# Optimization experiments

Measured on AMD Instinct MI355X. Metric: run time of the kernel, lower is better.

Reference implementation:

```python
import jax, jax.numpy as jnp
import numpy as np
import math

V, D, L, FF, H, DH, W, DM, T, B = 32000, 1024, 4, 4096, 16, 64, 256, 64, 1024, 1


def rms_norm(x, w):
    return x * jax.lax.rsqrt(jnp.mean(x * x, axis=-1, keepdims=True) + 1e-6) * w


def setup_inputs() -> dict:
    key = jax.random.key(0)
    ks = jax.random.split(key, 16)
    s = 0.02
    return {
        "x": jax.random.randint(ks[0], (B, T), 0, V),
        "embed": jax.random.normal(ks[1], (V, D), jnp.float32) * s,
        "ln_in_w": jnp.ones((D,), jnp.float32),
        "ln1_w": jnp.ones((L, D), jnp.float32),
        "lnd_w": jnp.ones((L, D), jnp.float32),
        "qkv_w": jax.random.normal(ks[2], (L, 3 * H * DH, D), jnp.float32) * s,
        "swa_out_w": jax.random.normal(ks[3], (L, D, H * DH), jnp.float32) * s,
        "k_w": jax.random.normal(ks[4], (L, H * DM, D), jnp.float32) * s,
        "v_w": jax.random.normal(ks[5], (L, H * DM, D), jnp.float32) * s,
        "q_w": jax.random.normal(ks[6], (L, H * DM, D), jnp.float32) * s,
        "beta_w": jax.random.normal(ks[7], (L, H, D), jnp.float32) * s,
        "mem_out_w": jax.random.normal(ks[8], (L, D, H * DM), jnp.float32) * s,
        "gate_w": jax.random.normal(ks[9], (L, D, D), jnp.float32) * s,
        "comb_w": jax.random.normal(ks[10], (L, D, D), jnp.float32) * s,
        "ln2_w": jnp.ones((L, D), jnp.float32),
        "wg": jax.random.normal(ks[11], (L, FF, D), jnp.float32) * s,
        "wu": jax.random.normal(ks[12], (L, FF, D), jnp.float32) * s,
        "wo": jax.random.normal(ks[13], (L, D, FF), jnp.float32) * s,
        "ln_out_w": jnp.ones((D,), jnp.float32),
    }


def _swa(h1, qkv_w, out_w):
    # h1: [B,T,D]
    qkv = jnp.einsum('btd,ed->bte', h1, qkv_w)  # [B,T,3*H*DH]
    q, k, v = jnp.split(qkv, 3, axis=-1)
    q = q.reshape(h1.shape[0], T, H, DH).transpose(0, 2, 1, 3)
    k = k.reshape(h1.shape[0], T, H, DH).transpose(0, 2, 1, 3)
    v = v.reshape(h1.shape[0], T, H, DH).transpose(0, 2, 1, 3)
    scores = jnp.einsum('bhqd,bhkd->bhqk', q, k) * (DH ** -0.5)
    pos = jnp.arange(T)
    dist = pos[:, None] - pos[None, :]
    allowed = (dist >= 0) & (dist < W)  # causal sliding window
    scores = jnp.where(allowed[None, None], scores, -jnp.inf)
    attn = jax.nn.softmax(scores, axis=-1)
    out = jnp.einsum('bhqk,bhkd->bhqd', attn, v)
    out = out.transpose(0, 2, 1, 3).reshape(h1.shape[0], T, H * DH)
    return jnp.einsum('bte,de->btd', out, out_w)


def _delta(h2, k_w, v_w, q_w, beta_w, mem_out_w):
    Bv = h2.shape[0]
    proj = lambda w: jnp.einsum('btd,ed->bte', h2, w).reshape(Bv, T, H, DM).transpose(0, 2, 1, 3)
    keys, values, queries = proj(k_w), proj(v_w), proj(q_w)
    beta = jax.nn.sigmoid(jnp.einsum('btd,hd->bht', h2, beta_w))  # [B,H,T]
    keys = keys / jnp.maximum(jnp.linalg.norm(keys, axis=-1, keepdims=True), 1e-12)
    queries = queries / jnp.maximum(jnp.linalg.norm(queries, axis=-1, keepdims=True), 1e-12)
    log_retain = jnp.log(1.0 - beta + 1e-8)
    cum_log = jnp.cumsum(log_retain, axis=-1)  # [B,H,T]
    log_decay = cum_log[..., :, None] - cum_log[..., None, :]  # [B,H,T,T]
    causal = jnp.triu(jnp.ones((T, T), dtype=bool))  # matches torch.triu mask in source
    decay = jnp.exp(jnp.minimum(log_decay, 0.0)) * causal
    kq = jnp.einsum('bhid,bhjd->bhij', queries, keys) / math.sqrt(DM)
    weights = kq * decay
    out = jnp.einsum('bhij,bhjd->bhid', weights, values)
    out = out + beta[..., None] * values
    out = out.transpose(0, 2, 1, 3).reshape(Bv, T, H * DM)
    return jnp.einsum('bte,de->btd', out, mem_out_w)


def reference(x, embed, ln_in_w, ln1_w, lnd_w, qkv_w, swa_out_w, k_w, v_w, q_w,
              beta_w, mem_out_w, gate_w, comb_w, ln2_w, wg, wu, wo, ln_out_w):
    h = rms_norm(embed[x], ln_in_w)  # [B,T,D]
    for l in range(L):
        h1 = rms_norm(h, ln1_w[l])
        h2 = rms_norm(h, lnd_w[l])
        local = _swa(h1, qkv_w[l], swa_out_w[l])
        global_ctx = _delta(h2, k_w[l], v_w[l], q_w[l], beta_w[l], mem_out_w[l])
        gate = jax.nn.sigmoid(jnp.einsum('btd,ed->bte', h1, gate_w[l]))
        mixed = jnp.einsum('btd,ed->bte', gate * local + (1.0 - gate) * global_ctx, comb_w[l])
        h = h + mixed
        hn = rms_norm(h, ln2_w[l])
        ffn = jnp.einsum('btf,df->btd', jax.nn.silu(jnp.einsum('btd,fd->btf', hn, wg[l])) * jnp.einsum('btd,fd->btf', hn, wu[l]), wo[l])
        h = h + ffn
    logits = jnp.einsum('btd,vd->btv', rms_norm(h, ln_out_w), embed)  # tied head
    return logits
```

## Files before the change

kernel.cpp:

```cpp
#include <hip/hip_runtime.h>

typedef unsigned short u16;
typedef unsigned int   u32;
typedef __attribute__((ext_vector_type(8))) __bf16 bfv8;
typedef __attribute__((ext_vector_type(4))) float  f32x4;
typedef __attribute__((ext_vector_type(4))) u32    u32x4;

__device__ __forceinline__ u16 f2bf(float f){
  u32 u = __builtin_bit_cast(u32, f);
  return (u16)((u + 0x7FFFu + ((u >> 16) & 1u)) >> 16);
}
__device__ __forceinline__ float bf2f(u16 b){
  return __builtin_bit_cast(float, ((u32)b) << 16);
}
__device__ __forceinline__ u32 pk2(float a, float b){
  return (u32)f2bf(a) | ((u32)f2bf(b) << 16);
}
__device__ __forceinline__ float wsum(float v){
  #pragma unroll
  for (int m = 32; m > 0; m >>= 1) v += __shfl_xor(v, m, 64);
  return v;
}
__device__ __forceinline__ void gload16(const void* g, void* l){
  __builtin_amdgcn_global_load_lds((const __attribute__((address_space(1))) void*)g,
                                   (__attribute__((address_space(3))) void*)l, 16, 0, 0);
}

struct CBatch { const float* s[12]; long long p4[13]; u16* dst; };
__global__ __launch_bounds__(256) void flm_conv(CBatch cb)
{
  const int seg = blockIdx.y;
  const long long base = cb.p4[seg];
  const long long n8 = (cb.p4[seg + 1] - base) >> 1;
  const f32x4* __restrict__ src = (const f32x4*)cb.s[seg];
  u32x4* __restrict__ dst = (u32x4*)cb.dst + (base >> 1);
  for (long long i = (long long)blockIdx.x * 256 + threadIdx.x; i < n8;
       i += (long long)gridDim.x * 256){
    f32x4 v0 = __builtin_nontemporal_load(src + 2*i);
    f32x4 v1 = __builtin_nontemporal_load(src + 2*i + 1);
    u32x4 p;
    p.x = pk2(v0.x, v0.y); p.y = pk2(v0.z, v0.w);
    p.z = pk2(v1.x, v1.y); p.w = pk2(v1.z, v1.w);
    __builtin_nontemporal_store(p, dst + i);
  }
}

struct GDesc {
  const u16* A; const float* Bw; float* Cf; u16* Cb;
  int lda, ldb, ldc, kbeg, kend, blk0, epi, pad;
};
struct GBatch { GDesc d[6]; int ng, total; };

template<bool BW>
__global__ __launch_bounds__(512) void flm_mgemm(GBatch gb)
{
  constexpr int LDK = BW ? 64 : 72;
  __shared__ u16 sA[128][LDK];
  __shared__ u16 sB[128][LDK];
  const int tid = threadIdx.x, lane = tid & 63, w = tid >> 6;

  const int T = gb.total, bid = blockIdx.x;
  const int q8 = T >> 3, r8 = T & 7, xc = bid & 7, of = bid >> 3;
  const int lin = (xc < r8 ? xc * (q8 + 1) : r8 * (q8 + 1) + (xc - r8) * q8) + of;
  int di = 0;
  #pragma unroll
  for (int i = 1; i < 6; i++) if (i < gb.ng && lin >= gb.d[i].blk0) di = i;
  const GDesc g = gb.d[di];
  const int local = lin - g.blk0;
  const int row0 = (local & 7) * 128;
  const int col0 = (local >> 3) * 128;
  const int wr = (w >> 2) * 64, wc = (w & 3) * 32;

  f32x4 acc[4][2];
  #pragma unroll
  for (int m = 0; m < 4; m++)
    #pragma unroll
    for (int n = 0; n < 2; n++)
      acc[m][n] = (f32x4){0.f, 0.f, 0.f, 0.f};

  const int csw = ((lane & 7) ^ (lane >> 3)) * 8;
  const u16* B16 = (const u16*)g.Bw;

  for (int k0 = g.kbeg; k0 < g.kend; k0 += 64){
    if constexpr (BW){
      const u16* a0 = g.A + (size_t)(row0 + w*16 + (lane>>3)) * g.lda + k0 + csw;
      const u16* b0 = B16 + (size_t)(col0 + w*16 + (lane>>3)) * g.ldb + k0 + csw;
      gload16(a0,                     &sA[w*16    ][0]);
      gload16(a0 + (size_t)8*g.lda,   &sA[w*16 + 8][0]);
      gload16(b0,                     &sB[w*16    ][0]);
      gload16(b0 + (size_t)8*g.ldb,   &sB[w*16 + 8][0]);
    } else {
      #pragma unroll
      for (int i = 0; i < 2; i++){
        int idx = tid + i * 512;
        int r = idx >> 3, c = (idx & 7) * 8;
        *(uint4*)&sA[r][c] = *(const uint4*)(g.A + (size_t)(row0 + r) * g.lda + k0 + c);
      }
      #pragma unroll
      for (int i = 0; i < 4; i++){
        int idx = tid + i * 512;
        int r = idx >> 4, c = (idx & 15) * 4;
        float4 v = *(const float4*)(g.Bw + (size_t)(col0 + r) * g.ldb + k0 + c);
        uint2 p; p.x = pk2(v.x, v.y); p.y = pk2(v.z, v.w);
        *(uint2*)&sB[r][c] = p;
      }
    }
    __syncthreads();
    #pragma unroll
    for (int kk = 0; kk < 2; kk++){
      bfv8 af[4], bfr[2];
      #pragma unroll
      for (int m = 0; m < 4; m++){
        int row = wr + m*16 + (lane & 15);
        if constexpr (BW){
          int slot = (kk*4 + (lane >> 4)) ^ (row & 7);
          af[m] = *(const bfv8*)((const char*)sA + row*128 + slot*16);
        } else {
          af[m] = *(const bfv8*)&sA[row][kk*32 + (lane >> 4) * 8];
        }
      }
      #pragma unroll
      for (int n = 0; n < 2; n++){
        int row = wc + n*16 + (lane & 15);
        if constexpr (BW){
          int slot = (kk*4 + (lane >> 4)) ^ (row & 7);
          bfr[n] = *(const bfv8*)((const char*)sB + row*128 + slot*16);
        } else {
          bfr[n] = *(const bfv8*)&sB[row][kk*32 + (lane >> 4) * 8];
        }
      }
      #pragma unroll
      for (int m = 0; m < 4; m++)
        #pragma unroll
        for (int n = 0; n < 2; n++)
          acc[m][n] = __builtin_amdgcn_mfma_f32_16x16x32_bf16(af[m], bfr[n], acc[m][n], 0, 0, 0);
    }
    __syncthreads();
  }

  #pragma unroll
  for (int m = 0; m < 4; m++){
    int rbase = row0 + wr + m*16 + (lane >> 4) * 4;
    #pragma unroll
    for (int n = 0; n < 2; n++){
      int col = col0 + wc + n*16 + (lane & 15);
      #pragma unroll
      for (int j = 0; j < 4; j++){
        float v = acc[m][n][j];
        size_t o = (size_t)(rbase + j) * g.ldc + col;
        switch (g.epi){
          case 0: g.Cf[o] = v; break;
          case 1: g.Cb[o] = f2bf(v); break;
          default: atomicAdd(&g.Cf[o], v); break;
        }
      }
    }
  }
}

__global__ __launch_bounds__(256) void flm_mix(
    const float* __restrict__ gr, const float* __restrict__ lo,
    const float* __restrict__ gl, u16* __restrict__ o)
{
  int i = blockIdx.x * 256 + threadIdx.x;
  float4 gv = ((const float4*)gr)[i];
  float4 lv = ((const float4*)lo)[i];
  float4 bv = ((const float4*)gl)[i];
  float sx = 1.f/(1.f+expf(-gv.x)), sy = 1.f/(1.f+expf(-gv.y));
  float sz = 1.f/(1.f+expf(-gv.z)), sw = 1.f/(1.f+expf(-gv.w));
  uint2 p;
  p.x = pk2(sx*lv.x + (1.f-sx)*bv.x, sy*lv.y + (1.f-sy)*bv.y);
  p.y = pk2(sz*lv.z + (1.f-sz)*bv.z, sw*lv.w + (1.f-sw)*bv.w);
  ((uint2*)o)[i] = p;
}

__global__ __launch_bounds__(256) void flm_silu(
    const u16* __restrict__ gg, const u16* __restrict__ uu, u16* __restrict__ o)
{
  int i = blockIdx.x * 256 + threadIdx.x;
  uint2 gv = ((const uint2*)gg)[i];
  uint2 uv = ((const uint2*)uu)[i];
  float g0 = bf2f((u16)gv.x), g1 = bf2f((u16)(gv.x >> 16));
  float g2 = bf2f((u16)gv.y), g3 = bf2f((u16)(gv.y >> 16));
  float u0 = bf2f((u16)uv.x), u1 = bf2f((u16)(uv.x >> 16));
  float u2 = bf2f((u16)uv.y), u3 = bf2f((u16)(uv.y >> 16));
  float a = g0 / (1.f + expf(-g0)) * u0;
  float b = g1 / (1.f + expf(-g1)) * u1;
  float c = g2 / (1.f + expf(-g2)) * u2;
  float d = g3 / (1.f + expf(-g3)) * u3;
  uint2 p; p.x = pk2(a, b); p.y = pk2(c, d);
  ((uint2*)o)[i] = p;
}

__global__ __launch_bounds__(256) void flm_embed(
    const int* __restrict__ x, const float* __restrict__ embed,
    const float* __restrict__ w, float* __restrict__ h)
{
  int t = blockIdx.x, tid = threadIdx.x;
  int tok = x[t];
  float4 v = ((const float4*)(embed + (size_t)tok * 1024))[tid];
  float ss = v.x*v.x + v.y*v.y + v.z*v.z + v.w*v.w;
  ss = wsum(ss);
  __shared__ float red[4];
  if ((tid & 63) == 0) red[tid >> 6] = ss;
  __syncthreads();
  float inv = rsqrtf((red[0]+red[1]+red[2]+red[3]) * (1.f/1024.f) + 1e-6f);
  float4 wv = ((const float4*)w)[tid];
  float4 o; o.x = v.x*inv*wv.x; o.y = v.y*inv*wv.y; o.z = v.z*inv*wv.z; o.w = v.w*inv*wv.w;
  ((float4*)(h + (size_t)t * 1024))[tid] = o;
}

__global__ __launch_bounds__(256) void flm_rms(
    const float* __restrict__ h, const float* __restrict__ w1, const float* __restrict__ w2,
    u16* __restrict__ o1, u16* __restrict__ o2)
{
  int t = blockIdx.x, tid = threadIdx.x;
  float4 v = ((const float4*)(h + (size_t)t * 1024))[tid];
  float ss = v.x*v.x + v.y*v.y + v.z*v.z + v.w*v.w;
  ss = wsum(ss);
  __shared__ float red[4];
  if ((tid & 63) == 0) red[tid >> 6] = ss;
  __syncthreads();
  float inv = rsqrtf((red[0]+red[1]+red[2]+red[3]) * (1.f/1024.f) + 1e-6f);
  {
    float4 wv = ((const float4*)w1)[tid];
    uint2 p; p.x = pk2(v.x*inv*wv.x, v.y*inv*wv.y); p.y = pk2(v.z*inv*wv.z, v.w*inv*wv.w);
    ((uint2*)(o1 + (size_t)t * 1024))[tid] = p;
  }
  if (o2 != nullptr){
    float4 wv = ((const float4*)w2)[tid];
    uint2 p; p.x = pk2(v.x*inv*wv.x, v.y*inv*wv.y); p.y = pk2(v.z*inv*wv.z, v.w*inv*wv.w);
    ((uint2*)(o2 + (size_t)t * 1024))[tid] = p;
  }
}

__global__ __launch_bounds__(64) void flm_betanorm(
    const u16* __restrict__ h2, const float* __restrict__ bw, float* __restrict__ beta,
    u16* __restrict__ keys, u16* __restrict__ queries)
{
  int t = blockIdx.x, lane = threadIdx.x;
  float hv[16];
  #pragma unroll
  for (int i = 0; i < 16; i++) hv[i] = bf2f(h2[(size_t)t*1024 + i*64 + lane]);
  for (int h = 0; h < 16; h++){
    float p = 0.f;
    #pragma unroll
    for (int i = 0; i < 16; i++) p += hv[i] * bw[h*1024 + i*64 + lane];
    p = wsum(p);
    if (lane == 0) beta[t*16 + h] = 1.f / (1.f + expf(-p));
  }
  #pragma unroll
  for (int h = 0; h < 16; h++){
    size_t idx = (size_t)t * 1024 + h * 64 + lane;
    float v = bf2f(keys[idx]);
    float nrm = fmaxf(sqrtf(wsum(v * v)), 1e-12f);
    keys[idx] = f2bf(v / nrm);
    float q = bf2f(queries[idx]);
    float qn = fmaxf(sqrtf(wsum(q * q)), 1e-12f);
    queries[idx] = f2bf(q / qn);
  }
}

__global__ __launch_bounds__(256) void flm_attn(
    const u16* __restrict__ qkv,
    const u16* __restrict__ keys, const u16* __restrict__ values, const u16* __restrict__ queries,
    const float* __restrict__ beta, u16* __restrict__ aout, u16* __restrict__ dout)
{
  __shared__ u16 sK[64][72];
  __shared__ u16 sVt[64][72];
  __shared__ u16 sP[4][16][72];
  const int tid = threadIdx.x, lane = tid & 63, w = tid >> 6;
  const int bx = blockIdx.x, h = blockIdx.y;
  const int base = h * 64;
  const int ri = w*16 + (lane>>4)*4;

  if (bx < 16){
    const int qt = bx;
    bfv8 aq[2];
    {
      int qrow = qt*64 + w*16 + (lane & 15);
      #pragma unroll
      for (int kk = 0; kk < 2; kk++)
        aq[kk] = *(const bfv8*)(qkv + (size_t)qrow*3072 + base + kk*32 + (lane>>4)*8);
    }
    f32x4 acc_o[4];
    float m_r[4], l_r[4];
    #pragma unroll
    for (int n = 0; n < 4; n++) acc_o[n] = (f32x4){0.f,0.f,0.f,0.f};
    #pragma unroll
    for (int r = 0; r < 4; r++){ m_r[r] = -1e30f; l_r[r] = 0.f; }
    const int jt0 = (qt >= 4) ? qt - 4 : 0;

    for (int jt = qt; jt >= jt0; jt--){
      #pragma unroll
      for (int i = 0; i < 2; i++){
        int idx = tid + i*256;
        int r = idx >> 3, c = (idx & 7) * 8;
        uint4 kv = *(const uint4*)(qkv + (size_t)(jt*64+r)*3072 + 1024 + base + c);
        *(uint4*)&sK[r][c] = kv;
        uint4 vv = *(const uint4*)(qkv + (size_t)(jt*64+r)*3072 + 2048 + base + c);
        u16 tmp[8]; *(uint4*)tmp = vv;
        #pragma unroll
        for (int e = 0; e < 8; e++) sVt[c+e][r] = tmp[e];
      }
      __syncthreads();

      f32x4 sv[4];
      #pragma unroll
      for (int n = 0; n < 4; n++) sv[n] = (f32x4){0.f,0.f,0.f,0.f};
      #pragma unroll
      for (int kk = 0; kk < 2; kk++){
        #pragma unroll
        for (int n = 0; n < 4; n++){
          bfv8 bk = *(const bfv8*)&sK[n*16 + (lane & 15)][(lane>>4)*8 + kk*32];
          sv[n] = __builtin_amdgcn_mfma_f32_16x16x32_bf16(aq[kk], bk, sv[n], 0, 0, 0);
        }
      }
      #pragma unroll
      for (int n = 0; n < 4; n++){
        int cj = n*16 + (lane & 15);
        #pragma unroll
        for (int r = 0; r < 4; r++){
          float s = sv[n][r] * 0.125f;
          if (jt == qt)      { if (cj > ri + r) s = -1e30f; }
          else if (jt == jt0 && qt - jt0 == 4) { if (cj <= ri + r) s = -1e30f; }
          sv[n][r] = s;
        }
      }
      float pv[4][4], scl[4];
      #pragma unroll
      for (int r = 0; r < 4; r++){
        float mx = -1e30f;
        #pragma unroll
        for (int n = 0; n < 4; n++) mx = fmaxf(mx, sv[n][r]);
        #pragma unroll
        for (int m = 1; m < 16; m <<= 1) mx = fmaxf(mx, __shfl_xor(mx, m, 64));
        float mn = fmaxf(m_r[r], mx);
        float sc = expf(m_r[r] - mn);
        m_r[r] = mn; scl[r] = sc;
        float rs = 0.f;
        #pragma unroll
        for (int n = 0; n < 4; n++){ float p = expf(sv[n][r] - mn); pv[n][r] = p; rs += p; }
        #pragma unroll
        for (int m = 1; m < 16; m <<= 1) rs += __shfl_xor(rs, m, 64);
        l_r[r] = l_r[r] * sc + rs;
      }
      #pragma unroll
      for (int n = 0; n < 4; n++){
        #pragma unroll
        for (int r = 0; r < 4; r++){
          acc_o[n][r] *= scl[r];
          sP[w][(lane>>4)*4 + r][n*16 + (lane & 15)] = f2bf(pv[n][r]);
        }
      }
      #pragma unroll
      for (int kk = 0; kk < 2; kk++){
        bfv8 ap = *(const bfv8*)&sP[w][lane & 15][(lane>>4)*8 + kk*32];
        #pragma unroll
        for (int n = 0; n < 4; n++){
          bfv8 bv = *(const bfv8*)&sVt[n*16 + (lane & 15)][(lane>>4)*8 + kk*32];
          acc_o[n] = __builtin_amdgcn_mfma_f32_16x16x32_bf16(ap, bv, acc_o[n], 0, 0, 0);
        }
      }
      __syncthreads();
    }

    #pragma unroll
    for (int n = 0; n < 4; n++){
      int col = base + n*16 + (lane & 15);
      #pragma unroll
      for (int r = 0; r < 4; r++){
        int row = qt*64 + ri + r;
        aout[(size_t)row*1024 + col] = f2bf(acc_o[n][r] / l_r[r]);
      }
    }
  } else {
    const int p = bx - 16;
    #pragma unroll 1
    for (int sel = 0; sel < 2; sel++){
      const int qt = sel ? (15 - p) : p;
      bfv8 aq[2];
      {
        int qrow = qt*64 + w*16 + (lane & 15);
        #pragma unroll
        for (int kk = 0; kk < 2; kk++)
          aq[kk] = *(const bfv8*)(queries + (size_t)qrow*1024 + base + kk*32 + (lane>>4)*8);
      }
      f32x4 acc_o[4];
      #pragma unroll
      for (int n = 0; n < 4; n++) acc_o[n] = (f32x4){0.f,0.f,0.f,0.f};

      for (int jt = qt; jt < 16; jt++){
        #pragma unroll
        for (int i = 0; i < 2; i++){
          int idx = tid + i*256;
          int r = idx >> 3, c = (idx & 7) * 8;
          uint4 kv = *(const uint4*)(keys + (size_t)(jt*64+r)*1024 + base + c);
          *(uint4*)&sK[r][c] = kv;
          uint4 vv = *(const uint4*)(values + (size_t)(jt*64+r)*1024 + base + c);
          u16 tmp[8]; *(uint4*)tmp = vv;
          #pragma unroll
          for (int e = 0; e < 8; e++) sVt[c+e][r] = tmp[e];
        }
        __syncthreads();

        f32x4 sv[4];
        #pragma unroll
        for (int n = 0; n < 4; n++) sv[n] = (f32x4){0.f,0.f,0.f,0.f};
        #pragma unroll
        for (int kk = 0; kk < 2; kk++){
          #pragma unroll
          for (int n = 0; n < 4; n++){
            bfv8 bk = *(const bfv8*)&sK[n*16 + (lane & 15)][(lane>>4)*8 + kk*32];
            sv[n] = __builtin_amdgcn_mfma_f32_16x16x32_bf16(aq[kk], bk, sv[n], 0, 0, 0);
          }
        }
        #pragma unroll
        for (int n = 0; n < 4; n++){
          int cj = n*16 + (lane & 15);
          #pragma unroll
          for (int r = 0; r < 4; r++){
            float pp = sv[n][r] * 0.125f;
            if (jt == qt && cj < ri + r) pp = 0.f;
            sP[w][(lane>>4)*4 + r][n*16 + (lane & 15)] = f2bf(pp);
          }
        }
        #pragma unroll
        for (int kk = 0; kk < 2; kk++){
          bfv8 ap = *(const bfv8*)&sP[w][lane & 15][(lane>>4)*8 + kk*32];
          #pragma unroll
          for (int n = 0; n < 4; n++){
            bfv8 bv = *(const bfv8*)&sVt[n*16 + (lane & 15)][(lane>>4)*8 + kk*32];
            acc_o[n] = __builtin_amdgcn_mfma_f32_16x16x32_bf16(ap, bv, acc_o[n], 0, 0, 0);
          }
        }
        __syncthreads();
      }

      #pragma unroll
      for (int n = 0; n < 4; n++){
        int col = base + n*16 + (lane & 15);
        #pragma unroll
        for (int r = 0; r < 4; r++){
          int row = qt*64 + ri + r;
          float b = beta[row*16 + h];
          float v = bf2f(values[(size_t)row*1024 + col]);
          dout[(size_t)row*1024 + col] = f2bf(acc_o[n][r] + b * v);
        }
      }
    }
  }
}

static GDesc mkd(const u16* A, int lda, const float* Bw, int ldb,
                 float* Cf, u16* Cb, int ldc,
                 int kbeg, int kend, int blk0, int epi){
  GDesc d; d.A=A; d.Bw=Bw; d.Cf=Cf; d.Cb=Cb;
  d.lda=lda; d.ldb=ldb; d.ldc=ldc; d.kbeg=kbeg; d.kend=kend; d.blk0=blk0; d.epi=epi; d.pad=0;
  return d;
}

extern "C" void kernel_launch(void* const* d_in, const int* in_sizes, int n_in,
                              void* d_out, int out_size, void* d_ws, size_t ws_size,
                              hipStream_t stream)
{
  (void)in_sizes; (void)n_in; (void)out_size;
  const int*   x        = (const int*)d_in[0];
  const float* embed    = (const float*)d_in[1];
  const float* ln_in_w  = (const float*)d_in[2];
  const float* ln1_w    = (const float*)d_in[3];
  const float* lnd_w    = (const float*)d_in[4];
  const float* qkv_w    = (const float*)d_in[5];
  const float* swa_out_w= (const float*)d_in[6];
  const float* k_w      = (const float*)d_in[7];
  const float* v_w      = (const float*)d_in[8];
  const float* q_w      = (const float*)d_in[9];
  const float* beta_w   = (const float*)d_in[10];
  const float* mem_out_w= (const float*)d_in[11];
  const float* gate_w   = (const float*)d_in[12];
  const float* comb_w   = (const float*)d_in[13];
  const float* ln2_w    = (const float*)d_in[14];
  const float* wg       = (const float*)d_in[15];
  const float* wu       = (const float*)d_in[16];
  const float* wo       = (const float*)d_in[17];
  const float* ln_out_w = (const float*)d_in[18];
  float* out = (float*)d_out;

  char* ws = (char*)d_ws;
  const size_t KB = 1024, MB = 1u << 20;
  float* h       = (float*)(ws + 0);
  u16*   h1      = (u16*)  (ws + 4*MB);
  u16*   h2      = (u16*)  (ws + 6*MB);
  u16*   qkvb    = (u16*)  (ws + 8*MB);
  u16*   keys    = (u16*)  (ws + 14*MB);
  u16*   values  = (u16*)  (ws + 16*MB);
  u16*   queries = (u16*)  (ws + 18*MB);
  float* beta    = (float*)(ws + 20*MB);
  u16*   attn    = (u16*)  (ws + 20*MB + 256*KB);
  u16*   delt    = (u16*)  (ws + 22*MB + 256*KB);
  float* localb  = (float*)(ws + 24*MB + 256*KB);
  float* globb   = (float*)(ws + 28*MB + 256*KB);
  float* gbuf    = (float*)(ws + 32*MB + 256*KB);
  u16*   mcomb   = (u16*)  (ws + 36*MB + 256*KB);
  u16*   hn      = (u16*)  (ws + 38*MB + 256*KB);
  u16*   g16     = (u16*)  (ws + 4*MB);
  u16*   u16b    = (u16*)  (ws + 12*MB);
  u16*   sbuf    = (u16*)  (ws + 20*MB);

  u16* wb = (u16*)(ws + 41*MB);
  size_t off = 0; auto nx = [&](size_t n){ size_t o = off; off += n; return o; };
  const size_t nEmb = 32768000ULL, nQkv = 12582912ULL, nSq = 4194304ULL, nFf = 16777216ULL;
  u16* wemb  = wb + nx(nEmb);
  u16* wqkv  = wb + nx(nQkv);
  u16* wswa  = wb + nx(nSq);
  u16* wk    = wb + nx(nSq);
  u16* wv    = wb + nx(nSq);
  u16* wq    = wb + nx(nSq);
  u16* wmem  = wb + nx(nSq);
  u16* wgate = wb + nx(nSq);
  u16* wcomb = wb + nx(nSq);
  u16* wwg   = wb + nx(nFf);
  u16* wwu   = wb + nx(nFf);
  u16* wwo   = wb + nx(nFf);
  const size_t NEED = 41*MB + off * 2;
  const bool bw = (ws_size >= NEED);

  auto MG = [&](int nblk, GBatch& gbv){
    if (bw) flm_mgemm<true><<<nblk, 512, 0, stream>>>(gbv);
    else    flm_mgemm<false><<<nblk, 512, 0, stream>>>(gbv);
  };

  if (bw){
    CBatch cb;
    const float* srcs[12] = {embed, qkv_w, swa_out_w, k_w, v_w, q_w,
                             mem_out_w, gate_w, comb_w, wg, wu, wo};
    const size_t ns[12] = {nEmb, nQkv, nSq, nSq, nSq, nSq, nSq, nSq, nSq, nFf, nFf, nFf};
    long long acc4 = 0;
    for (int i = 0; i < 12; i++){ cb.s[i] = srcs[i]; cb.p4[i] = acc4; acc4 += (long long)(ns[i] >> 2); }
    cb.p4[12] = acc4; cb.dst = wb;
    flm_conv<<<dim3(1024, 12), 256, 0, stream>>>(cb);
  }

  flm_embed<<<1024, 256, 0, stream>>>(x, embed, ln_in_w, h);

  for (int l = 0; l < 4; l++){
    const size_t lq = (size_t)l * 3145728, ls = (size_t)l * 1048576, lf = (size_t)l * 4194304;
    const float* Wqkv  = bw ? (const float*)(wqkv  + lq) : qkv_w     + lq;
    const float* Wk    = bw ? (const float*)(wk    + ls) : k_w       + ls;
    const float* Wv    = bw ? (const float*)(wv    + ls) : v_w       + ls;
    const float* Wq    = bw ? (const float*)(wq    + ls) : q_w       + ls;
    const float* Wswa  = bw ? (const float*)(wswa  + ls) : swa_out_w + ls;
    const float* Wmem  = bw ? (const float*)(wmem  + ls) : mem_out_w + ls;
    const float* Wgate = bw ? (const float*)(wgate + ls) : gate_w    + ls;
    const float* Wcomb = bw ? (const float*)(wcomb + ls) : comb_w    + ls;
    const float* Wwg   = bw ? (const float*)(wwg   + lf) : wg        + lf;
    const float* Wwu   = bw ? (const float*)(wwu   + lf) : wu        + lf;
    const float* Wwo   = bw ? (const float*)(wwo   + lf) : wo        + lf;

    flm_rms<<<1024, 256, 0, stream>>>(h, ln1_w + l*1024, lnd_w + l*1024, h1, h2);

    {
      GBatch gb;
      gb.d[0] = mkd(h1, 1024, Wqkv, 1024, nullptr, qkvb, 3072, 0, 1024, 0, 1);
      gb.d[1] = mkd(h2, 1024, Wk, 1024, nullptr, keys, 1024, 0, 1024, 192, 1);
      gb.d[2] = mkd(h2, 1024, Wv, 1024, nullptr, values, 1024, 0, 1024, 256, 1);
      gb.d[3] = mkd(h2, 1024, Wq, 1024, nullptr, queries, 1024, 0, 1024, 320, 1);
      gb.d[4] = mkd(h1, 1024, Wgate, 1024, gbuf, nullptr, 1024, 0, 1024, 384, 0);
      gb.d[5] = gb.d[4]; gb.d[5].blk0 = 0x7fffffff;
      gb.ng = 5; gb.total = 448;
      MG(448, gb);
    }
    flm_betanorm<<<1024, 64, 0, stream>>>(h2, beta_w + (size_t)l*16*1024, beta, keys, queries);
    flm_attn<<<dim3(24, 16), 256, 0, stream>>>(qkvb, keys, values, queries, beta, attn, delt);

    {
      GBatch gb;
      gb.d[0] = mkd(attn, 1024, Wswa, 1024, localb, nullptr, 1024, 0, 1024, 0, 0);
      gb.d[1] = mkd(delt, 1024, Wmem, 1024, globb, nullptr, 1024, 0, 1024, 64, 0);
      gb.d[2] = gb.d[1]; gb.d[2].blk0 = 0x7fffffff;
      gb.d[3] = gb.d[2]; gb.d[4] = gb.d[2]; gb.d[5] = gb.d[2];
      gb.ng = 2; gb.total = 128;
      MG(128, gb);
    }
    flm_mix<<<1024, 256, 0, stream>>>(gbuf, localb, globb, mcomb);
    {
      GBatch gb;
      gb.d[0] = mkd(mcomb, 1024, Wcomb, 1024, h, nullptr, 1024, 0, 512, 0, 5);
      gb.d[1] = mkd(mcomb, 1024, Wcomb, 1024, h, nullptr, 1024, 512, 1024, 64, 5);
      gb.d[2] = gb.d[1]; gb.d[2].blk0 = 0x7fffffff;
      gb.d[3] = gb.d[2]; gb.d[4] = gb.d[2]; gb.d[5] = gb.d[2];
      gb.ng = 2; gb.total = 128;
      MG(128, gb);
    }
    flm_rms<<<1024, 256, 0, stream>>>(h, ln2_w + l*1024, nullptr, hn, nullptr);
    {
      GBatch gb;
      gb.d[0] = mkd(hn, 1024, Wwg, 1024, nullptr, g16, 4096, 0, 1024, 0, 1);
      gb.d[1] = mkd(hn, 1024, Wwu, 1024, nullptr, u16b, 4096, 0, 1024, 256, 1);
      gb.d[2] = gb.d[1]; gb.d[2].blk0 = 0x7fffffff;
      gb.d[3] = gb.d[2]; gb.d[4] = gb.d[2]; gb.d[5] = gb.d[2];
      gb.ng = 2; gb.total = 512;
      MG(512, gb);
    }
    flm_silu<<<4096, 256, 0, stream>>>(g16, u16b, sbuf);
    {
      GBatch gb;
      for (int s = 0; s < 4; s++)
        gb.d[s] = mkd(sbuf, 4096, Wwo, 4096, h, nullptr, 1024, s*1024, (s+1)*1024, s*64, 5);
      gb.d[4] = gb.d[3]; gb.d[4].blk0 = 0x7fffffff;
      gb.d[5] = gb.d[4];
      gb.ng = 4; gb.total = 256;
      MG(256, gb);
    }
  }

  flm_rms<<<1024, 256, 0, stream>>>(h, ln_out_w, nullptr, hn, nullptr);
  {
    GBatch gb;
    gb.d[0] = mkd(hn, 1024, bw ? (const float*)wemb : embed, 1024, out, nullptr, 32000,
                  0, 1024, 0, 0);
    gb.d[1] = gb.d[0]; gb.d[1].blk0 = 0x7fffffff;
    gb.d[2] = gb.d[1]; gb.d[3] = gb.d[1]; gb.d[4] = gb.d[1]; gb.d[5] = gb.d[1];
    gb.ng = 1; gb.total = 2000;
    MG(2000, gb);
  }
}
```

Baseline: 1.069 ms.

## Rebalance launches: split-K out-projections, move gate GEMM, one attention block per tile

```diff
diff --git a/kernel.cpp b/kernel.cpp
--- a/kernel.cpp
+++ b/kernel.cpp
@@ -158,6 +158,24 @@
   }
 }
 
+__global__ __launch_bounds__(256) void flm_mix5(
+    const float* __restrict__ gr, const float* __restrict__ lo0, const float* __restrict__ lo1,
+    const float* __restrict__ gl0, const float* __restrict__ gl1, u16* __restrict__ o)
+{
+  int i = blockIdx.x * 256 + threadIdx.x;
+  float4 gv = ((const float4*)gr)[i];
+  float4 l0 = ((const float4*)lo0)[i];
+  float4 l1 = ((const float4*)lo1)[i];
+  float4 b0 = ((const float4*)gl0)[i];
+  float4 b1 = ((const float4*)gl1)[i];
+  float sx = 1.f/(1.f+expf(-gv.x)), sy = 1.f/(1.f+expf(-gv.y));
+  float sz = 1.f/(1.f+expf(-gv.z)), sw = 1.f/(1.f+expf(-gv.w));
+  uint2 p;
+  p.x = pk2(sx*(l0.x+l1.x) + (1.f-sx)*(b0.x+b1.x), sy*(l0.y+l1.y) + (1.f-sy)*(b0.y+b1.y));
+  p.y = pk2(sz*(l0.z+l1.z) + (1.f-sz)*(b0.z+b1.z), sw*(l0.w+l1.w) + (1.f-sw)*(b0.w+b1.w));
+  ((uint2*)o)[i] = p;
+}
+
 __global__ __launch_bounds__(256) void flm_mix(
     const float* __restrict__ gr, const float* __restrict__ lo,
     const float* __restrict__ gl, u16* __restrict__ o)
@@ -270,12 +288,11 @@
   __shared__ u16 sVt[64][72];
   __shared__ u16 sP[4][16][72];
   const int tid = threadIdx.x, lane = tid & 63, w = tid >> 6;
-  const int bx = blockIdx.x, h = blockIdx.y;
+  const int qt = blockIdx.x, h = blockIdx.y;
   const int base = h * 64;
   const int ri = w*16 + (lane>>4)*4;
 
-  if (bx < 16){
-    const int qt = bx;
+  if (blockIdx.z == 0){
     bfv8 aq[2];
     {
       int qrow = qt*64 + w*16 + (lane & 15);
@@ -375,78 +392,73 @@
       }
     }
   } else {
-    const int p = bx - 16;
-    #pragma unroll 1
-    for (int sel = 0; sel < 2; sel++){
-      const int qt = sel ? (15 - p) : p;
-      bfv8 aq[2];
-      {
-        int qrow = qt*64 + w*16 + (lane & 15);
-        #pragma unroll
-        for (int kk = 0; kk < 2; kk++)
-          aq[kk] = *(const bfv8*)(queries + (size_t)qrow*1024 + base + kk*32 + (lane>>4)*8);
-      }
-      f32x4 acc_o[4];
-      #pragma unroll
-      for (int n = 0; n < 4; n++) acc_o[n] = (f32x4){0.f,0.f,0.f,0.f};
-
-      for (int jt = qt; jt < 16; jt++){
-        #pragma unroll
-        for (int i = 0; i < 2; i++){
-          int idx = tid + i*256;
-          int r = idx >> 3, c = (idx & 7) * 8;
-          uint4 kv = *(const uint4*)(keys + (size_t)(jt*64+r)*1024 + base + c);
-          *(uint4*)&sK[r][c] = kv;
-          uint4 vv = *(const uint4*)(values + (size_t)(jt*64+r)*1024 + base + c);
-          u16 tmp[8]; *(uint4*)tmp = vv;
-          #pragma unroll
-          for (int e = 0; e < 8; e++) sVt[c+e][r] = tmp[e];
-        }
-        __syncthreads();
-
-        f32x4 sv[4];
-        #pragma unroll
-        for (int n = 0; n < 4; n++) sv[n] = (f32x4){0.f,0.f,0.f,0.f};
-        #pragma unroll
-        for (int kk = 0; kk < 2; kk++){
-          #pragma unroll
-          for (int n = 0; n < 4; n++){
-            bfv8 bk = *(const bfv8*)&sK[n*16 + (lane & 15)][(lane>>4)*8 + kk*32];
-            sv[n] = __builtin_amdgcn_mfma_f32_16x16x32_bf16(aq[kk], bk, sv[n], 0, 0, 0);
-          }
-        }
+    bfv8 aq[2];
+    {
+      int qrow = qt*64 + w*16 + (lane & 15);
+      #pragma unroll
+      for (int kk = 0; kk < 2; kk++)
+        aq[kk] = *(const bfv8*)(queries + (size_t)qrow*1024 + base + kk*32 + (lane>>4)*8);
+    }
+    f32x4 acc_o[4];
+    #pragma unroll
+    for (int n = 0; n < 4; n++) acc_o[n] = (f32x4){0.f,0.f,0.f,0.f};
+
+    for (int jt = qt; jt < 16; jt++){
+      #pragma unroll
+      for (int i = 0; i < 2; i++){
+        int idx = tid + i*256;
+        int r = idx >> 3, c = (idx & 7) * 8;
+        uint4 kv = *(const uint4*)(keys + (size_t)(jt*64+r)*1024 + base + c);
+        *(uint4*)&sK[r][c] = kv;
+        uint4 vv = *(const uint4*)(values + (size_t)(jt*64+r)*1024 + base + c);
+        u16 tmp[8]; *(uint4*)tmp = vv;
+        #pragma unroll
+        for (int e = 0; e < 8; e++) sVt[c+e][r] = tmp[e];
+      }
+      __syncthreads();
+
+      f32x4 sv[4];
+      #pragma unroll
+      for (int n = 0; n < 4; n++) sv[n] = (f32x4){0.f,0.f,0.f,0.f};
+      #pragma unroll
+      for (int kk = 0; kk < 2; kk++){
         #pragma unroll
         for (int n = 0; n < 4; n++){
-          int cj = n*16 + (lane & 15);
-          #pragma unroll
-          for (int r = 0; r < 4; r++){
-            float pp = sv[n][r] * 0.125f;
-            if (jt == qt && cj < ri + r) pp = 0.f;
-            sP[w][(lane>>4)*4 + r][n*16 + (lane & 15)] = f2bf(pp);
-          }
-        }
-        #pragma unroll
-        for (int kk = 0; kk < 2; kk++){
-          bfv8 ap = *(const bfv8*)&sP[w][lane & 15][(lane>>4)*8 + kk*32];
-          #pragma unroll
-          for (int n = 0; n < 4; n++){
-            bfv8 bv = *(const bfv8*)&sVt[n*16 + (lane & 15)][(lane>>4)*8 + kk*32];
-            acc_o[n] = __builtin_amdgcn_mfma_f32_16x16x32_bf16(ap, bv, acc_o[n], 0, 0, 0);
-          }
-        }
-        __syncthreads();
-      }
-
+          bfv8 bk = *(const bfv8*)&sK[n*16 + (lane & 15)][(lane>>4)*8 + kk*32];
+          sv[n] = __builtin_amdgcn_mfma_f32_16x16x32_bf16(aq[kk], bk, sv[n], 0, 0, 0);
+        }
+      }
       #pragma unroll
       for (int n = 0; n < 4; n++){
-        int col = base + n*16 + (lane & 15);
+        int cj = n*16 + (lane & 15);
         #pragma unroll
         for (int r = 0; r < 4; r++){
-          int row = qt*64 + ri + r;
-          float b = beta[row*16 + h];
-          float v = bf2f(values[(size_t)row*1024 + col]);
-          dout[(size_t)row*1024 + col] = f2bf(acc_o[n][r] + b * v);
-        }
+          float p = sv[n][r] * 0.125f;
+          if (jt == qt && cj < ri + r) p = 0.f;
+          sP[w][(lane>>4)*4 + r][n*16 + (lane & 15)] = f2bf(p);
+        }
+      }
+      #pragma unroll
+      for (int kk = 0; kk < 2; kk++){
+        bfv8 ap = *(const bfv8*)&sP[w][lane & 15][(lane>>4)*8 + kk*32];
+        #pragma unroll
+        for (int n = 0; n < 4; n++){
+          bfv8 bv = *(const bfv8*)&sVt[n*16 + (lane & 15)][(lane>>4)*8 + kk*32];
+          acc_o[n] = __builtin_amdgcn_mfma_f32_16x16x32_bf16(ap, bv, acc_o[n], 0, 0, 0);
+        }
+      }
+      __syncthreads();
+    }
+
+    #pragma unroll
+    for (int n = 0; n < 4; n++){
+      int col = base + n*16 + (lane & 15);
+      #pragma unroll
+      for (int r = 0; r < 4; r++){
+        int row = qt*64 + ri + r;
+        float b = beta[row*16 + h];
+        float v = bf2f(values[(size_t)row*1024 + col]);
+        dout[(size_t)row*1024 + col] = f2bf(acc_o[n][r] + b * v);
       }
     }
   }
@@ -498,16 +510,18 @@
   float* beta    = (float*)(ws + 20*MB);
   u16*   attn    = (u16*)  (ws + 20*MB + 256*KB);
   u16*   delt    = (u16*)  (ws + 22*MB + 256*KB);
-  float* localb  = (float*)(ws + 24*MB + 256*KB);
-  float* globb   = (float*)(ws + 28*MB + 256*KB);
-  float* gbuf    = (float*)(ws + 32*MB + 256*KB);
-  u16*   mcomb   = (u16*)  (ws + 36*MB + 256*KB);
-  u16*   hn      = (u16*)  (ws + 38*MB + 256*KB);
+  float* lo0     = (float*)(ws + 24*MB + 256*KB);
+  float* lo1     = (float*)(ws + 28*MB + 256*KB);
+  float* gl0     = (float*)(ws + 32*MB + 256*KB);
+  float* gl1     = (float*)(ws + 36*MB + 256*KB);
+  float* gbuf    = (float*)(ws + 40*MB + 256*KB);
+  u16*   mcomb   = (u16*)  (ws + 44*MB + 256*KB);
+  u16*   hn      = (u16*)  (ws + 46*MB + 256*KB);
   u16*   g16     = (u16*)  (ws + 4*MB);
   u16*   u16b    = (u16*)  (ws + 12*MB);
   u16*   sbuf    = (u16*)  (ws + 20*MB);
 
-  u16* wb = (u16*)(ws + 41*MB);
+  u16* wb = (u16*)(ws + 48*MB + 512*KB);
   size_t off = 0; auto nx = [&](size_t n){ size_t o = off; off += n; return o; };
   const size_t nEmb = 32768000ULL, nQkv = 12582912ULL, nSq = 4194304ULL, nFf = 16777216ULL;
   u16* wemb  = wb + nx(nEmb);
@@ -522,7 +536,7 @@
   u16* wwg   = wb + nx(nFf);
   u16* wwu   = wb + nx(nFf);
   u16* wwo   = wb + nx(nFf);
-  const size_t NEED = 41*MB + off * 2;
+  const size_t NEED = 48*MB + 512*KB + off * 2;
   const bool bw = (ws_size >= NEED);
 
   auto MG = [&](int nblk, GBatch& gbv){
@@ -565,24 +579,43 @@
       gb.d[1] = mkd(h2, 1024, Wk, 1024, nullptr, keys, 1024, 0, 1024, 192, 1);
       gb.d[2] = mkd(h2, 1024, Wv, 1024, nullptr, values, 1024, 0, 1024, 256, 1);
       gb.d[3] = mkd(h2, 1024, Wq, 1024, nullptr, queries, 1024, 0, 1024, 320, 1);
-      gb.d[4] = mkd(h1, 1024, Wgate, 1024, gbuf, nullptr, 1024, 0, 1024, 384, 0);
+      if (bw){
+        gb.d[4] = gb.d[3]; gb.d[4].blk0 = 0x7fffffff;
+        gb.d[5] = gb.d[4];
+        gb.ng = 4; gb.total = 384;
+        MG(384, gb);
+      } else {
+        gb.d[4] = mkd(h1, 1024, Wgate, 1024, gbuf, nullptr, 1024, 0, 1024, 384, 0);
+        gb.d[5] = gb.d[4]; gb.d[5].blk0 = 0x7fffffff;
+        gb.ng = 5; gb.total = 448;
+        MG(448, gb);
+      }
+    }
+    flm_betanorm<<<1024, 64, 0, stream>>>(h2, beta_w + (size_t)l*16*1024, beta, keys, queries);
+    flm_attn<<<dim3(16, 16, 2), 256, 0, stream>>>(qkvb, keys, values, queries, beta, attn, delt);
+
+    if (bw){
+      GBatch gb;
+      gb.d[0] = mkd(attn, 1024, Wswa, 1024, lo0, nullptr, 1024, 0,   512,  0,   0);
+      gb.d[1] = mkd(attn, 1024, Wswa, 1024, lo1, nullptr, 1024, 512, 1024, 64,  0);
+      gb.d[2] = mkd(delt, 1024, Wmem, 1024, gl0, nullptr, 1024, 0,   512,  128, 0);
+      gb.d[3] = mkd(delt, 1024, Wmem, 1024, gl1, nullptr, 1024, 512, 1024, 192, 0);
+      gb.d[4] = mkd(h1,   1024, Wgate,1024, gbuf,nullptr, 1024, 0,  1024,  256, 0);
       gb.d[5] = gb.d[4]; gb.d[5].blk0 = 0x7fffffff;
-      gb.ng = 5; gb.total = 448;
-      MG(448, gb);
-    }
-    flm_betanorm<<<1024, 64, 0, stream>>>(h2, beta_w + (size_t)l*16*1024, beta, keys, queries);
-    flm_attn<<<dim3(24, 16), 256, 0, stream>>>(qkvb, keys, values, queries, beta, attn, delt);
-
-    {
+      gb.ng = 5; gb.total = 320;
+      MG(320, gb);
+      flm_mix5<<<1024, 256, 0, stream>>>(gbuf, lo0, lo1, gl0, gl1, mcomb);
+    } else {
       GBatch gb;
-      gb.d[0] = mkd(attn, 1024, Wswa, 1024, localb, nullptr, 1024, 0, 1024, 0, 0);
-      gb.d[1] = mkd(delt, 1024, Wmem, 1024, globb, nullptr, 1024, 0, 1024, 64, 0);
+      gb.d[0] = mkd(attn, 1024, Wswa, 1024, lo0, nullptr, 1024, 0, 1024, 0, 0);
+      gb.d[1] = mkd(delt, 1024, Wmem, 1024, gl0, nullptr, 1024, 0, 1024, 64, 0);
       gb.d[2] = gb.d[1]; gb.d[2].blk0 = 0x7fffffff;
       gb.d[3] = gb.d[2]; gb.d[4] = gb.d[2]; gb.d[5] = gb.d[2];
       gb.ng = 2; gb.total = 128;
       MG(128, gb);
-    }
-    flm_mix<<<1024, 256, 0, stream>>>(gbuf, localb, globb, mcomb);
+      flm_mix<<<1024, 256, 0, stream>>>(gbuf, lo0, gl0, mcomb);
+    }
+
     {
       GBatch gb;
       gb.d[0] = mkd(mcomb, 1024, Wcomb, 1024, h, nullptr, 1024, 0, 512, 0, 5);
```

Result: faster. 1.028 ms (-3.8%).

## Emit transposed V from GEMM epilogue and split attention grid by branch

Applied to the files above, without the earlier changes.

```diff
diff --git a/kernel.cpp b/kernel.cpp
--- a/kernel.cpp
+++ b/kernel.cpp
@@ -144,14 +144,21 @@
     #pragma unroll
     for (int n = 0; n < 2; n++){
       int col = col0 + wc + n*16 + (lane & 15);
-      #pragma unroll
-      for (int j = 0; j < 4; j++){
-        float v = acc[m][n][j];
-        size_t o = (size_t)(rbase + j) * g.ldc + col;
-        switch (g.epi){
-          case 0: g.Cf[o] = v; break;
-          case 1: g.Cb[o] = f2bf(v); break;
-          default: atomicAdd(&g.Cf[o], v); break;
+      if (g.epi == 2){
+        uint2 p;
+        p.x = pk2(acc[m][n][0], acc[m][n][1]);
+        p.y = pk2(acc[m][n][2], acc[m][n][3]);
+        *(uint2*)&g.Cb[(size_t)col * g.ldc + rbase] = p;
+      } else {
+        #pragma unroll
+        for (int j = 0; j < 4; j++){
+          float v = acc[m][n][j];
+          size_t o = (size_t)(rbase + j) * g.ldc + col;
+          switch (g.epi){
+            case 0: g.Cf[o] = v; break;
+            case 1: g.Cb[o] = f2bf(v); break;
+            default: atomicAdd(&g.Cf[o], v); break;
+          }
         }
       }
     }
@@ -262,26 +269,25 @@
 }
 
 __global__ __launch_bounds__(256) void flm_attn(
-    const u16* __restrict__ qkv,
-    const u16* __restrict__ keys, const u16* __restrict__ values, const u16* __restrict__ queries,
+    const u16* __restrict__ qkvb, const u16* __restrict__ qvT,
+    const u16* __restrict__ keys, const u16* __restrict__ valT, const u16* __restrict__ queries,
     const float* __restrict__ beta, u16* __restrict__ aout, u16* __restrict__ dout)
 {
   __shared__ u16 sK[64][72];
   __shared__ u16 sVt[64][72];
   __shared__ u16 sP[4][16][72];
   const int tid = threadIdx.x, lane = tid & 63, w = tid >> 6;
-  const int bx = blockIdx.x, h = blockIdx.y;
+  const int qt = blockIdx.x, h = blockIdx.y;
   const int base = h * 64;
   const int ri = w*16 + (lane>>4)*4;
 
-  if (bx < 16){
-    const int qt = bx;
+  if (blockIdx.z == 0){
     bfv8 aq[2];
     {
       int qrow = qt*64 + w*16 + (lane & 15);
       #pragma unroll
       for (int kk = 0; kk < 2; kk++)
-        aq[kk] = *(const bfv8*)(qkv + (size_t)qrow*3072 + base + kk*32 + (lane>>4)*8);
+        aq[kk] = *(const bfv8*)(qkvb + (size_t)qrow*2048 + base + kk*32 + (lane>>4)*8);
     }
     f32x4 acc_o[4];
     float m_r[4], l_r[4];
@@ -296,12 +302,8 @@
       for (int i = 0; i < 2; i++){
         int idx = tid + i*256;
         int r = idx >> 3, c = (idx & 7) * 8;
-        uint4 kv = *(const uint4*)(qkv + (size_t)(jt*64+r)*3072 + 1024 + base + c);
-        *(uint4*)&sK[r][c] = kv;
-        uint4 vv = *(const uint4*)(qkv + (size_t)(jt*64+r)*3072 + 2048 + base + c);
-        u16 tmp[8]; *(uint4*)tmp = vv;
-        #pragma unroll
-        for (int e = 0; e < 8; e++) sVt[c+e][r] = tmp[e];
+        *(uint4*)&sK[r][c] = *(const uint4*)(qkvb + (size_t)(jt*64+r)*2048 + 1024 + base + c);
+        *(uint4*)&sVt[r][c] = *(const uint4*)(qvT + (size_t)(base + r)*1024 + jt*64 + c);
       }
       __syncthreads();
 
@@ -375,78 +377,69 @@
       }
     }
   } else {
-    const int p = bx - 16;
-    #pragma unroll 1
-    for (int sel = 0; sel < 2; sel++){
-      const int qt = sel ? (15 - p) : p;
-      bfv8 aq[2];
-      {
-        int qrow = qt*64 + w*16 + (lane & 15);
-        #pragma unroll
-        for (int kk = 0; kk < 2; kk++)
-          aq[kk] = *(const bfv8*)(queries + (size_t)qrow*1024 + base + kk*32 + (lane>>4)*8);
-      }
-      f32x4 acc_o[4];
-      #pragma unroll
-      for (int n = 0; n < 4; n++) acc_o[n] = (f32x4){0.f,0.f,0.f,0.f};
-
-      for (int jt = qt; jt < 16; jt++){
-        #pragma unroll
-        for (int i = 0; i < 2; i++){
-          int idx = tid + i*256;
-          int r = idx >> 3, c = (idx & 7) * 8;
-          uint4 kv = *(const uint4*)(keys + (size_t)(jt*64+r)*1024 + base + c);
-          *(uint4*)&sK[r][c] = kv;
-          uint4 vv = *(const uint4*)(values + (size_t)(jt*64+r)*1024 + base + c);
-          u16 tmp[8]; *(uint4*)tmp = vv;
-          #pragma unroll
-          for (int e = 0; e < 8; e++) sVt[c+e][r] = tmp[e];
-        }
-        __syncthreads();
-
-        f32x4 sv[4];
-        #pragma unroll
-        for (int n = 0; n < 4; n++) sv[n] = (f32x4){0.f,0.f,0.f,0.f};
-        #pragma unroll
-        for (int kk = 0; kk < 2; kk++){
-          #pragma unroll
-          for (int n = 0; n < 4; n++){
-            bfv8 bk = *(const bfv8*)&sK[n*16 + (lane & 15)][(lane>>4)*8 + kk*32];
-            sv[n] = __builtin_amdgcn_mfma_f32_16x16x32_bf16(aq[kk], bk, sv[n], 0, 0, 0);
-          }
-        }
+    bfv8 aq[2];
+    {
+      int qrow = qt*64 + w*16 + (lane & 15);
+      #pragma unroll
+      for (int kk = 0; kk < 2; kk++)
+        aq[kk] = *(const bfv8*)(queries + (size_t)qrow*1024 + base + kk*32 + (lane>>4)*8);
+    }
+    f32x4 acc_o[4];
+    #pragma unroll
+    for (int n = 0; n < 4; n++) acc_o[n] = (f32x4){0.f,0.f,0.f,0.f};
+
+    for (int jt = qt; jt < 16; jt++){
+      #pragma unroll
+      for (int i = 0; i < 2; i++){
+        int idx = tid + i*256;
+        int r = idx >> 3, c = (idx & 7) * 8;
+        *(uint4*)&sK[r][c] = *(const uint4*)(keys + (size_t)(jt*64+r)*1024 + base + c);
+        *(uint4*)&sVt[r][c] = *(const uint4*)(valT + (size_t)(base + r)*1024 + jt*64 + c);
+      }
+      __syncthreads();
+
+      f32x4 sv[4];
+      #pragma unroll
+      for (int n = 0; n < 4; n++) sv[n] = (f32x4){0.f,0.f,0.f,0.f};
+      #pragma unroll
+      for (int kk = 0; kk < 2; kk++){
         #pragma unroll
         for (int n = 0; n < 4; n++){
-          int cj = n*16 + (lane & 15);
-          #pragma unroll
-          for (int r = 0; r < 4; r++){
-            float pp = sv[n][r] * 0.125f;
-            if (jt == qt && cj < ri + r) pp = 0.f;
-            sP[w][(lane>>4)*4 + r][n*16 + (lane & 15)] = f2bf(pp);
-          }
-        }
-        #pragma unroll
-        for (int kk = 0; kk < 2; kk++){
-          bfv8 ap = *(const bfv8*)&sP[w][lane & 15][(lane>>4)*8 + kk*32];
-          #pragma unroll
-          for (int n = 0; n < 4; n++){
-            bfv8 bv = *(const bfv8*)&sVt[n*16 + (lane & 15)][(lane>>4)*8 + kk*32];
-            acc_o[n] = __builtin_amdgcn_mfma_f32_16x16x32_bf16(ap, bv, acc_o[n], 0, 0, 0);
-          }
-        }
-        __syncthreads();
-      }
-
+          bfv8 bk = *(const bfv8*)&sK[n*16 + (lane & 15)][(lane>>4)*8 + kk*32];
+          sv[n] = __builtin_amdgcn_mfma_f32_16x16x32_bf16(aq[kk], bk, sv[n], 0, 0, 0);
+        }
+      }
       #pragma unroll
       for (int n = 0; n < 4; n++){
-        int col = base + n*16 + (lane & 15);
+        int cj = n*16 + (lane & 15);
         #pragma unroll
         for (int r = 0; r < 4; r++){
-          int row = qt*64 + ri + r;
-          float b = beta[row*16 + h];
-          float v = bf2f(values[(size_t)row*1024 + col]);
-          dout[(size_t)row*1024 + col] = f2bf(acc_o[n][r] + b * v);
-        }
+          float p = sv[n][r] * 0.125f;
+          if (jt == qt && cj < ri + r) p = 0.f;
+          sP[w][(lane>>4)*4 + r][n*16 + (lane & 15)] = f2bf(p);
+        }
+      }
+      #pragma unroll
+      for (int kk = 0; kk < 2; kk++){
+        bfv8 ap = *(const bfv8*)&sP[w][lane & 15][(lane>>4)*8 + kk*32];
+        #pragma unroll
+        for (int n = 0; n < 4; n++){
+          bfv8 bv = *(const bfv8*)&sVt[n*16 + (lane & 15)][(lane>>4)*8 + kk*32];
+          acc_o[n] = __builtin_amdgcn_mfma_f32_16x16x32_bf16(ap, bv, acc_o[n], 0, 0, 0);
+        }
+      }
+      __syncthreads();
+    }
+
+    #pragma unroll
+    for (int n = 0; n < 4; n++){
+      int col = base + n*16 + (lane & 15);
+      #pragma unroll
+      for (int r = 0; r < 4; r++){
+        int row = qt*64 + ri + r;
+        float b = beta[row*16 + h];
+        float v = bf2f(valT[(size_t)col*1024 + row]);
+        dout[(size_t)row*1024 + col] = f2bf(acc_o[n][r] + b * v);
       }
     }
   }
@@ -492,14 +485,15 @@
   u16*   h1      = (u16*)  (ws + 4*MB);
   u16*   h2      = (u16*)  (ws + 6*MB);
   u16*   qkvb    = (u16*)  (ws + 8*MB);
+  u16*   qvT     = (u16*)  (ws + 12*MB);
   u16*   keys    = (u16*)  (ws + 14*MB);
-  u16*   values  = (u16*)  (ws + 16*MB);
+  u16*   valT    = (u16*)  (ws + 16*MB);
   u16*   queries = (u16*)  (ws + 18*MB);
   float* beta    = (float*)(ws + 20*MB);
   u16*   attn    = (u16*)  (ws + 20*MB + 256*KB);
   u16*   delt    = (u16*)  (ws + 22*MB + 256*KB);
-  float* localb  = (float*)(ws + 24*MB + 256*KB);
-  float* globb   = (float*)(ws + 28*MB + 256*KB);
+  float* lo0     = (float*)(ws + 24*MB + 256*KB);
+  float* gl0     = (float*)(ws + 28*MB + 256*KB);
   float* gbuf    = (float*)(ws + 32*MB + 256*KB);
   u16*   mcomb   = (u16*)  (ws + 36*MB + 256*KB);
   u16*   hn      = (u16*)  (ws + 38*MB + 256*KB);
@@ -546,6 +540,7 @@
   for (int l = 0; l < 4; l++){
     const size_t lq = (size_t)l * 3145728, ls = (size_t)l * 1048576, lf = (size_t)l * 4194304;
     const float* Wqkv  = bw ? (const float*)(wqkv  + lq) : qkv_w     + lq;
+    const float* WqkvV = bw ? (const float*)(wqkv  + lq + 2048*1024ULL) : qkv_w + lq + 2048*1024ULL;
     const float* Wk    = bw ? (const float*)(wk    + ls) : k_w       + ls;
     const float* Wv    = bw ? (const float*)(wv    + ls) : v_w       + ls;
     const float* Wq    = bw ? (const float*)(wq    + ls) : q_w       + ls;
@@ -561,28 +556,28 @@
 
     {
       GBatch gb;
-      gb.d[0] = mkd(h1, 1024, Wqkv, 1024, nullptr, qkvb, 3072, 0, 1024, 0, 1);
-      gb.d[1] = mkd(h2, 1024, Wk, 1024, nullptr, keys, 1024, 0, 1024, 192, 1);
-      gb.d[2] = mkd(h2, 1024, Wv, 1024, nullptr, values, 1024, 0, 1024, 256, 1);
-      gb.d[3] = mkd(h2, 1024, Wq, 1024, nullptr, queries, 1024, 0, 1024, 320, 1);
-      gb.d[4] = mkd(h1, 1024, Wgate, 1024, gbuf, nullptr, 1024, 0, 1024, 384, 0);
-      gb.d[5] = gb.d[4]; gb.d[5].blk0 = 0x7fffffff;
-      gb.ng = 5; gb.total = 448;
+      gb.d[0] = mkd(h1, 1024, Wqkv,  1024, nullptr, qkvb,    2048, 0, 1024, 0,   1);
+      gb.d[1] = mkd(h1, 1024, WqkvV, 1024, nullptr, qvT,     1024, 0, 1024, 128, 2);
+      gb.d[2] = mkd(h2, 1024, Wk,    1024, nullptr, keys,    1024, 0, 1024, 192, 1);
+      gb.d[3] = mkd(h2, 1024, Wv,    1024, nullptr, valT,    1024, 0, 1024, 256, 2);
+      gb.d[4] = mkd(h2, 1024, Wq,    1024, nullptr, queries, 1024, 0, 1024, 320, 1);
+      gb.d[5] = mkd(h1, 1024, Wgate, 1024, gbuf,    nullptr, 1024, 0, 1024, 384, 0);
+      gb.ng = 6; gb.total = 448;
       MG(448, gb);
     }
     flm_betanorm<<<1024, 64, 0, stream>>>(h2, beta_w + (size_t)l*16*1024, beta, keys, queries);
-    flm_attn<<<dim3(24, 16), 256, 0, stream>>>(qkvb, keys, values, queries, beta, attn, delt);
+    flm_attn<<<dim3(16, 16, 2), 256, 0, stream>>>(qkvb, qvT, keys, valT, queries, beta, attn, delt);
 
     {
       GBatch gb;
-      gb.d[0] = mkd(attn, 1024, Wswa, 1024, localb, nullptr, 1024, 0, 1024, 0, 0);
-      gb.d[1] = mkd(delt, 1024, Wmem, 1024, globb, nullptr, 1024, 0, 1024, 64, 0);
+      gb.d[0] = mkd(attn, 1024, Wswa, 1024, lo0, nullptr, 1024, 0, 1024, 0, 0);
+      gb.d[1] = mkd(delt, 1024, Wmem, 1024, gl0, nullptr, 1024, 0, 1024, 64, 0);
       gb.d[2] = gb.d[1]; gb.d[2].blk0 = 0x7fffffff;
       gb.d[3] = gb.d[2]; gb.d[4] = gb.d[2]; gb.d[5] = gb.d[2];
       gb.ng = 2; gb.total = 128;
       MG(128, gb);
     }
-    flm_mix<<<1024, 256, 0, stream>>>(gbuf, localb, globb, mcomb);
+    flm_mix<<<1024, 256, 0, stream>>>(gbuf, lo0, gl0, mcomb);
     {
       GBatch gb;
       gb.d[0] = mkd(mcomb, 1024, Wcomb, 1024, h, nullptr, 1024, 0, 512, 0, 5);
```

After: 1.001 ms. -6.4%, faster.
